# Performance work log

Hardware: AMD Instinct MI355X
Metric: run time of the kernel (lower is better)

Reference implementation:

```python
import jax, jax.numpy as jnp
import numpy as np

G, N = 1024, 40            # graphs, nodes per graph (complete graphs)
SLOPE = 0.1                # leaky relu negative slope
SMAT_IDX = jnp.array([0, 1, 2, 3, 1, 4, 5, 6, 2, 5, 7, 8, 3, 6, 8, 9])


def setup_inputs() -> dict:
    key = jax.random.key(0)
    ks = jax.random.split(key, 24)

    # --- graph structure: G identical complete graphs of N nodes ---
    ii, jj = np.meshgrid(np.arange(N), np.arange(N), indexing="ij")
    mask = ii != jj
    src_l, dst_l = ii[mask], jj[mask]              # directed edges per graph
    offs = (np.arange(G) * N)[:, None]
    edge_index = np.stack([(src_l[None] + offs).ravel(),
                           (dst_l[None] + offs).ravel()]).astype(np.int64)
    iu, ju = np.triu_indices(N, 1)
    M = iu.shape[0]                                 # 780 undirected edges
    ud_edges = np.stack([iu, ju], 1).astype(np.int64)
    edge_map = np.zeros((N, N), np.int64)
    edge_map[iu, ju] = np.arange(M)
    edge_map[ju, iu] = np.arange(M)

    def w(k, shape, fan_in):
        return jax.random.normal(k, shape, jnp.float32) / np.sqrt(fan_in)

    inp = {
        "x": jax.random.normal(ks[0], (G * N, 16), jnp.float32),
        "edge_index": jnp.asarray(edge_index),
        "ud_edges": jnp.asarray(ud_edges),
        "edge_map": jnp.asarray(edge_map),
        # GCN stack 6->32->32->64
        "Wg0": w(ks[1], (6, 32), 6),   "bg0": jnp.zeros((32,), jnp.float32),
        "Wg1": w(ks[2], (32, 32), 32), "bg1": jnp.zeros((32,), jnp.float32),
        "Wg2": w(ks[3], (32, 64), 32), "bg2": jnp.zeros((64,), jnp.float32),
        # node MLP 64->64->64->10
        "Wn0": w(ks[4], (64, 64), 64), "bn0": jnp.zeros((64,), jnp.float32),
        "Wn1": w(ks[5], (64, 64), 64), "bn1": jnp.zeros((64,), jnp.float32),
        "Wn2": w(ks[6], (64, 10), 64), "bn2": jnp.zeros((10,), jnp.float32),
        # edge MLP 64->64->64->10
        "We0": w(ks[7], (64, 64), 64), "be0": jnp.zeros((64,), jnp.float32),
        "We1": w(ks[8], (64, 64), 64), "be1": jnp.zeros((64,), jnp.float32),
        "We2": w(ks[9], (64, 10), 64), "be2": jnp.zeros((10,), jnp.float32),
    }
    return inp


def _forward(x, edge_index, ud_edges, edge_map,
             Wg0, bg0, Wg1, bg1, Wg2, bg2,
             Wn0, bn0, Wn1, bn1, Wn2, bn2,
             We0, be0, We1, be1, We2, be2):
    num_nodes = x.shape[0]
    h = x[:, :6]                                   # node_feature_mode == 1
    src, dst = edge_index[0], edge_index[1]

    # GCN normalization (add_self_loops=False, edge_weight=1)
    deg = jax.ops.segment_sum(jnp.ones(src.shape[0], x.dtype), dst,
                              num_segments=num_nodes)
    dis = jnp.where(deg > 0, jax.lax.rsqrt(jnp.maximum(deg, 1e-12)), 0.0)
    norm = dis[src] * dis[dst]                     # [E]

    def gcn(h, W, b):
        m = (h @ W)[src] * norm[:, None]
        return jax.ops.segment_sum(m, dst, num_segments=num_nodes) + b

    # eval mode: dropout is identity
    h = jax.nn.leaky_relu(gcn(h, Wg0, bg0), SLOPE)
    h = jax.nn.leaky_relu(gcn(h, Wg1, bg1), SLOPE)
    h = gcn(h, Wg2, bg2)                           # [G*N, 64]

    hg = h.reshape(G, N, -1)                       # [G, N, 64]

    def mlp(z, Ws, bs):
        for W, b in zip(Ws[:-1], bs[:-1]):
            z = jax.nn.leaky_relu(z @ W + b, SLOPE)
        return z @ Ws[-1] + bs[-1]

    vp = mlp(hg, [Wn0, Wn1, Wn2], [bn0, bn1, bn2])            # [G, N, 10]
    e = hg[:, ud_edges[:, 0], :] + hg[:, ud_edges[:, 1], :]   # [G, M, 64]
    ep = mlp(e, [We0, We1, We2], [be0, be1, be2])             # [G, M, 10]

    # recover_X: diag blocks smat(vp[i]), off-diag smat(ep[edge_map[i,j]])
    epm = ep[:, edge_map, :]                                  # [G, N, N, 10]
    eye = jnp.eye(N, dtype=bool)[None, :, :, None]
    vecs = jnp.where(eye, vp[:, :, None, :], epm)             # [G, N, N, 10]
    blocks = vecs[..., SMAT_IDX].reshape(G, N, N, 4, 4)
    X = blocks.transpose(0, 1, 3, 2, 4).reshape(G, 4 * N, 4 * N)
    return h, X


def reference(x, edge_index, ud_edges, edge_map,
              Wg0, bg0, Wg1, bg1, Wg2, bg2,
              Wn0, bn0, Wn1, bn1, Wn2, bn2,
              We0, be0, We1, be1, We2, be2):
    return _forward(x, edge_index, ud_edges, edge_map,
                    Wg0, bg0, Wg1, bg1, Wg2, bg2,
                    Wn0, bn0, Wn1, bn1, Wn2, bn2,
                    We0, be0, We1, be1, We2, be2)
```

## Files before the change

### kernel.cpp

```cpp
#include <hip/hip_runtime.h>

#define G_GRAPHS 1024
#define N_NODES  40
#define M_EDGES  780
#define NUM_NODES (G_GRAPHS * N_NODES)
#define H_ELEMS  (NUM_NODES * 64)
#define X_STRIDE 160
#define X_PER_G  25600
#define SLOPE 0.1f

#define PACK_PER_MLP 9216

typedef __bf16 bf16x8 __attribute__((ext_vector_type(8)));
typedef unsigned short us8 __attribute__((ext_vector_type(8)));
typedef float f32x4 __attribute__((ext_vector_type(4)));

__device__ __forceinline__ float lrelu(float v) { return fmaxf(v, SLOPE * v); }
__device__ __forceinline__ unsigned short f2bf(float x) {
    __bf16 b = (__bf16)x;
    return __builtin_bit_cast(unsigned short, b);
}
__device__ __forceinline__ unsigned int pk2bf(float a, float b) {
    return (unsigned int)f2bf(a) | ((unsigned int)f2bf(b) << 16);
}

__global__ __launch_bounds__(256) void k_prep(const float* __restrict__ We0,
                                              const float* __restrict__ We1,
                                              const float* __restrict__ We2,
                                              const float* __restrict__ Wn0,
                                              const float* __restrict__ Wn1,
                                              const float* __restrict__ Wn2,
                                              unsigned short* __restrict__ wp) {
    int t = blockIdx.x * 256 + threadIdx.x;
    int mlp = t / PACK_PER_MLP;
    int o = t - mlp * PACK_PER_MLP;
    const float* W0 = mlp ? Wn0 : We0;
    const float* W1 = mlp ? Wn1 : We1;
    const float* W2 = mlp ? Wn2 : We2;
    float val;
    if (o < 8192) {
        const float* W = (o < 4096) ? W0 : W1;
        int idx = o & 4095;
        int j = idx & 7, l = (idx >> 3) & 63, tt = idx >> 9;
        int kt = tt & 1, mt = tt >> 1;
        int k = kt * 32 + ((l >> 4) & 3) * 8 + j;
        int m = mt * 16 + (l & 15);
        val = W[k * 64 + m];
    } else {
        int idx = o - 8192;
        int j = idx & 7, l = (idx >> 3) & 63, kt = idx >> 9;
        int k = kt * 32 + ((l >> 4) & 3) * 8 + j;
        int m = l & 15;
        val = (m < 10) ? W2[k * 10 + m] : 0.f;
    }
    wp[mlp * PACK_PER_MLP + o] = f2bf(val);
}

struct ChunkRegs {
    bf16x8 A1[4][2];
    bf16x8 A2[4][2];
    bf16x8 A3[2];
    float4 bv0[4];
    float4 bv1[4];
    float  bz[4];
};

__device__ __forceinline__ void run_pair(int R0A, int R0B, int w, int l,
                                         const float4* sh4,
                                         unsigned short* sBA,
                                         unsigned short* sBB,
                                         float* sEP,
                                         const unsigned short* sIJ,
                                         const ChunkRegs& cr) {
    const int nl = l & 15;
    const int rq = (l >> 4) & 3;
    const int rl = l >> 1;
    const int hf2 = l & 1;

    auto decode = [&](int row, int& ii, int& jj, bool& is_e, bool& is_n) {
        is_e = (row < 780);
        is_n = (row >= 800 && row < 840);
        ii = 0; jj = 0;
        if (is_e) {
            unsigned short e = sIJ[row];
            ii = e >> 8; jj = e & 255;
        } else if (is_n) {
            ii = jj = row - 800;
        }
    };
    int iiA, jjA, iiB, jjB; bool ieA, inA, ieB, inB;
    decode(R0A + rl, iiA, jjA, ieA, inA);
    decode(R0B + rl, iiB, jjB, ieB, inB);

    auto ebuild = [&](unsigned short* sB, int ii, int jj, bool is_e) {
        unsigned short tmp[32];
#pragma unroll
        for (int q = 0; q < 8; q++) {
            int u = hf2 * 8 + q;
            float4 a = sh4[ii * 16 + (u ^ ((ii & 7) << 1))];
            if (is_e) {
                float4 bq = sh4[jj * 16 + (u ^ ((jj & 7) << 1))];
                a.x += bq.x; a.y += bq.y; a.z += bq.z; a.w += bq.w;
            }
            tmp[4 * q + 0] = f2bf(a.x); tmp[4 * q + 1] = f2bf(a.y);
            tmp[4 * q + 2] = f2bf(a.z); tmp[4 * q + 3] = f2bf(a.w);
        }
        int r_sb = 32 * w + rl;
#pragma unroll
        for (int q = 0; q < 4; q++) {
            int cs = (hf2 * 4 + q) ^ (r_sb & 7);
            *(us8*)((char*)sB + r_sb * 128 + cs * 16) = *(const us8*)(tmp + 8 * q);
        }
    };
    ebuild(sBA, iiA, jjA, ieA);
    ebuild(sBB, iiB, jjB, ieB);

    auto ZB = [&](const unsigned short* s, int nt, int kt) -> bf16x8 {
        int node = 32 * w + nt * 16 + nl;
        int cs = (kt * 4 + rq) ^ (node & 7);
        return __builtin_bit_cast(bf16x8,
            *(const us8*)((const char*)s + node * 128 + cs * 16));
    };
    auto zstore = [&](unsigned short* s, int mt, int nt, const f32x4& v) {
        int node = 32 * w + nt * 16 + nl;
        int cs = (mt * 2 + (rq >> 1)) ^ (node & 7);
        uint2 u = make_uint2(pk2bf(v[0], v[1]), pk2bf(v[2], v[3]));
        *(uint2*)((char*)s + node * 128 + cs * 16 + (rq & 1) * 8) = u;
    };

    auto gemm_layer = [&](unsigned short* s, const bf16x8 A[4][2],
                          const float4* bv) {
        bf16x8 B[2][2];
#pragma unroll
        for (int nt = 0; nt < 2; nt++)
#pragma unroll
            for (int kt = 0; kt < 2; kt++) B[nt][kt] = ZB(s, nt, kt);
#pragma unroll
        for (int mt = 0; mt < 4; mt++) {
            float4 b = bv[mt];
#pragma unroll
            for (int nt = 0; nt < 2; nt++) {
                f32x4 acc = (f32x4){b.x, b.y, b.z, b.w};
                acc = __builtin_amdgcn_mfma_f32_16x16x32_bf16(A[mt][0], B[nt][0], acc, 0, 0, 0);
                acc = __builtin_amdgcn_mfma_f32_16x16x32_bf16(A[mt][1], B[nt][1], acc, 0, 0, 0);
                f32x4 z;
                z[0] = lrelu(acc[0]); z[1] = lrelu(acc[1]);
                z[2] = lrelu(acc[2]); z[3] = lrelu(acc[3]);
                zstore(s, mt, nt, z);
            }
        }
    };

    gemm_layer(sBA, cr.A1, cr.bv0);
    gemm_layer(sBB, cr.A1, cr.bv0);
    gemm_layer(sBA, cr.A2, cr.bv1);
    gemm_layer(sBB, cr.A2, cr.bv1);

    auto gemm3 = [&](unsigned short* s, int R0) {
        bf16x8 B[2][2];
#pragma unroll
        for (int nt = 0; nt < 2; nt++)
#pragma unroll
            for (int kt = 0; kt < 2; kt++) B[nt][kt] = ZB(s, nt, kt);
#pragma unroll
        for (int nt = 0; nt < 2; nt++) {
            f32x4 acc = (f32x4){cr.bz[0], cr.bz[1], cr.bz[2], cr.bz[3]};
            acc = __builtin_amdgcn_mfma_f32_16x16x32_bf16(cr.A3[0], B[nt][0], acc, 0, 0, 0);
            acc = __builtin_amdgcn_mfma_f32_16x16x32_bf16(cr.A3[1], B[nt][1], acc, 0, 0, 0);
            int rowe = R0 + nt * 16 + nl;
            bool valid = (rowe < 780) || (rowe >= 800 && rowe < 840);
            if (valid && rq < 3) {
                int epr = (rowe < 780) ? rowe : rowe - 20;
                float* p = sEP + epr * 10 + rq * 4;
                *(float2*)p = make_float2(acc[0], acc[1]);
                if (rq < 2)
                    *(float2*)(p + 2) = make_float2(acc[2], acc[3]);
            }
        }
    };
    gemm3(sBA, R0A);
    gemm3(sBB, R0B);
}

__device__ __forceinline__ void run_single(int R0, int w, int l,
                                           const float4* sh4,
                                           unsigned short* sBA,
                                           float* sEP,
                                           const unsigned short* sIJ,
                                           const ChunkRegs& cr) {
    const int nl = l & 15;
    const int rq = (l >> 4) & 3;
    const int rl = l >> 1;
    const int hf2 = l & 1;
    const int row = R0 + rl;

    const bool is_e = (row < 780);
    const bool is_n = (row >= 800 && row < 840);
    int ii = 0, jj = 0;
    if (is_e) {
        unsigned short e = sIJ[row];
        ii = e >> 8; jj = e & 255;
    } else if (is_n) {
        ii = jj = row - 800;
    }

    {
        unsigned short tmp[32];
#pragma unroll
        for (int q = 0; q < 8; q++) {
            int u = hf2 * 8 + q;
            float4 a = sh4[ii * 16 + (u ^ ((ii & 7) << 1))];
            if (is_e) {
                float4 bq = sh4[jj * 16 + (u ^ ((jj & 7) << 1))];
                a.x += bq.x; a.y += bq.y; a.z += bq.z; a.w += bq.w;
            }
            tmp[4 * q + 0] = f2bf(a.x); tmp[4 * q + 1] = f2bf(a.y);
            tmp[4 * q + 2] = f2bf(a.z); tmp[4 * q + 3] = f2bf(a.w);
        }
        int r_sb = 32 * w + rl;
#pragma unroll
        for (int q = 0; q < 4; q++) {
            int cs = (hf2 * 4 + q) ^ (r_sb & 7);
            *(us8*)((char*)sBA + r_sb * 128 + cs * 16) = *(const us8*)(tmp + 8 * q);
        }
    }

    auto ZB = [&](int nt, int kt) -> bf16x8 {
        int node = 32 * w + nt * 16 + nl;
        int cs = (kt * 4 + rq) ^ (node & 7);
        return __builtin_bit_cast(bf16x8,
            *(const us8*)((const char*)sBA + node * 128 + cs * 16));
    };
    auto zstore = [&](int mt, int nt, const f32x4& v) {
        int node = 32 * w + nt * 16 + nl;
        int cs = (mt * 2 + (rq >> 1)) ^ (node & 7);
        uint2 u = make_uint2(pk2bf(v[0], v[1]), pk2bf(v[2], v[3]));
        *(uint2*)((char*)sBA + node * 128 + cs * 16 + (rq & 1) * 8) = u;
    };
    auto gemm_layer = [&](const bf16x8 A[4][2], const float4* bv) {
        bf16x8 B[2][2];
#pragma unroll
        for (int nt = 0; nt < 2; nt++)
#pragma unroll
            for (int kt = 0; kt < 2; kt++) B[nt][kt] = ZB(nt, kt);
#pragma unroll
        for (int mt = 0; mt < 4; mt++) {
            float4 b = bv[mt];
#pragma unroll
            for (int nt = 0; nt < 2; nt++) {
                f32x4 acc = (f32x4){b.x, b.y, b.z, b.w};
                acc = __builtin_amdgcn_mfma_f32_16x16x32_bf16(A[mt][0], B[nt][0], acc, 0, 0, 0);
                acc = __builtin_amdgcn_mfma_f32_16x16x32_bf16(A[mt][1], B[nt][1], acc, 0, 0, 0);
                f32x4 z;
                z[0] = lrelu(acc[0]); z[1] = lrelu(acc[1]);
                z[2] = lrelu(acc[2]); z[3] = lrelu(acc[3]);
                zstore(mt, nt, z);
            }
        }
    };
    gemm_layer(cr.A1, cr.bv0);
    gemm_layer(cr.A2, cr.bv1);
    {
        bf16x8 B[2][2];
#pragma unroll
        for (int nt = 0; nt < 2; nt++)
#pragma unroll
            for (int kt = 0; kt < 2; kt++) B[nt][kt] = ZB(nt, kt);
#pragma unroll
        for (int nt = 0; nt < 2; nt++) {
            f32x4 acc = (f32x4){cr.bz[0], cr.bz[1], cr.bz[2], cr.bz[3]};
            acc = __builtin_amdgcn_mfma_f32_16x16x32_bf16(cr.A3[0], B[nt][0], acc, 0, 0, 0);
            acc = __builtin_amdgcn_mfma_f32_16x16x32_bf16(cr.A3[1], B[nt][1], acc, 0, 0, 0);
            int rowe = R0 + nt * 16 + nl;
            bool valid = (rowe < 780) || (rowe >= 800 && rowe < 840);
            if (valid && rq < 3) {
                int epr = (rowe < 780) ? rowe : rowe - 20;
                float* p = sEP + epr * 10 + rq * 4;
                *(float2*)p = make_float2(acc[0], acc[1]);
                if (rq < 2)
                    *(float2*)(p + 2) = make_float2(acc[2], acc[3]);
            }
        }
    }
}

__global__ __launch_bounds__(256, 2) void k_fused(const float* __restrict__ x,
                                                  const float* __restrict__ Wg0,
                                                  const float* __restrict__ bg0,
                                                  const float* __restrict__ Wg1,
                                                  const float* __restrict__ bg1,
                                                  const float* __restrict__ Wg2,
                                                  const float* __restrict__ bg2,
                                                  const unsigned short* __restrict__ wp,
                                                  const float* __restrict__ be0,
                                                  const float* __restrict__ be1,
                                                  const float* __restrict__ be2,
                                                  const float* __restrict__ bn0,
                                                  const float* __restrict__ bn1,
                                                  const float* __restrict__ bn2,
                                                  float* __restrict__ hout,
                                                  float* __restrict__ X) {
    __shared__ __align__(16) char smem[77368];
    float* sh           = (float*)smem;
    unsigned short* sBA = (unsigned short*)(smem + 10240);
    unsigned short* sBB = (unsigned short*)(smem + 26624);
    float* sEP          = (float*)(smem + 43008);
    unsigned short* sIJ = (unsigned short*)(smem + 75808);
    float* h0  = (float*)smem;
    float* h1  = (float*)(smem + 20480);
    float* h2  = (float*)(smem + 26624);
    float* P   = (float*)(smem + 43008);

    const int g = blockIdx.x;
    const int tid = threadIdx.x;
    const int l = tid & 63;
    const int w = tid >> 6;
    const float inv39 = 1.0f / 39.0f;
    const int c32 = tid & 31;
    const int c64 = tid & 63;
    const int rq = (l >> 4) & 3;

    for (int m = tid; m < 780; m += 256) {
        float tq = 6241.0f - 8.0f * (float)m;
        int i0 = (int)(0.5f * (79.0f - sqrtf(tq)));
        i0 = min(38, max(0, i0));
        int cum = 39 * i0 - ((i0 * (i0 - 1)) >> 1);
        if (cum > m) { --i0; cum = 39 * i0 - ((i0 * (i0 - 1)) >> 1); }
        else if (m - cum >= 39 - i0) { cum += 39 - i0; ++i0; }
        int jj = i0 + 1 + (m - cum);
        sIJ[m] = (unsigned short)((i0 << 8) | jj);
    }

    {
        float w0c[6], w1c[32], w2c[32];
#pragma unroll
        for (int f = 0; f < 6; f++)  w0c[f] = Wg0[f * 32 + c32];
#pragma unroll
        for (int m = 0; m < 32; m++) w1c[m] = Wg1[m * 32 + c32];
#pragma unroll
        for (int m = 0; m < 32; m++) w2c[m] = Wg2[m * 64 + c64];
        const float b0c = bg0[c32];
        const float b1c = bg1[c32];
        const float b2c = bg2[c64];

        if (tid < 240) {
            int n = tid / 6, f = tid - n * 6;
            h0[tid] = x[(g * N_NODES + n) * 16 + f];
        }
        __syncthreads();

        float breg[10];
        const int n0 = tid >> 5;

        {
            float psum = 0.f;
#pragma unroll
            for (int t = 0; t < 5; t++) {
                int n = n0 + 8 * t;
                float s = 0.f;
#pragma unroll
                for (int f = 0; f < 6; f++) s += h0[n * 6 + f] * w0c[f];
                breg[t] = s; psum += s;
            }
            P[n0 * 32 + c32] = psum;
        }
        __syncthreads();
        {
            float s0 = 0.f;
#pragma unroll
            for (int grp = 0; grp < 8; grp++) s0 += P[grp * 32 + c32];
#pragma unroll
            for (int t = 0; t < 5; t++)
                h1[(n0 + 8 * t) * 32 + c32] = lrelu((s0 - breg[t]) * inv39 + b0c);
        }
        __syncthreads();

        {
            float psum = 0.f;
#pragma unroll
            for (int t = 0; t < 5; t++) {
                int n = n0 + 8 * t;
                const float4* hp = (const float4*)(h1 + n * 32);
                float s = 0.f;
#pragma unroll
                for (int q = 0; q < 8; q++) {
                    float4 hv = hp[q];
                    s += hv.x * w1c[4 * q + 0] + hv.y * w1c[4 * q + 1]
                       + hv.z * w1c[4 * q + 2] + hv.w * w1c[4 * q + 3];
                }
                breg[t] = s; psum += s;
            }
            P[n0 * 32 + c32] = psum;
        }
        __syncthreads();
        {
            float s0 = 0.f;
#pragma unroll
            for (int grp = 0; grp < 8; grp++) s0 += P[grp * 32 + c32];
#pragma unroll
            for (int t = 0; t < 5; t++)
                h2[(n0 + 8 * t) * 32 + c32] = lrelu((s0 - breg[t]) * inv39 + b1c);
        }
        __syncthreads();

        const int n02 = tid >> 6;
        {
            float psum = 0.f;
#pragma unroll
            for (int t = 0; t < 10; t++) {
                int n = n02 + 4 * t;
                const float4* hp = (const float4*)(h2 + n * 32);
                float s = 0.f;
#pragma unroll
                for (int q = 0; q < 8; q++) {
                    float4 hv = hp[q];
                    s += hv.x * w2c[4 * q + 0] + hv.y * w2c[4 * q + 1]
                       + hv.z * w2c[4 * q + 2] + hv.w * w2c[4 * q + 3];
                }
                breg[t] = s; psum += s;
            }
            P[n02 * 64 + c64] = psum;
        }
        __syncthreads();
        {
            float s0 = 0.f;
#pragma unroll
            for (int grp = 0; grp < 4; grp++) s0 += P[grp * 64 + c64];
#pragma unroll
            for (int t = 0; t < 10; t++) {
                int n = n02 + 4 * t;
                float v = (s0 - breg[t]) * inv39 + b2c;
                hout[g * N_NODES * 64 + n * 64 + c64] = v;
                int u = c64 >> 2;
                int us = u ^ ((n & 7) << 1);
                sh[n * 64 + us * 4 + (c64 & 3)] = v;
            }
        }
    }
    __syncthreads();

    const float4* sh4 = (const float4*)sh;

    auto WA = [&](const unsigned short* base, int mt, int kt) -> bf16x8 {
        return __builtin_bit_cast(bf16x8,
            *(const us8*)(base + ((mt * 2 + kt) * 64 + l) * 8));
    };
    auto loadW = [&](ChunkRegs& cr, const unsigned short* wb,
                     const float* B0, const float* B1, const float* B2) {
#pragma unroll
        for (int mt = 0; mt < 4; mt++) {
#pragma unroll
            for (int kt = 0; kt < 2; kt++) {
                cr.A1[mt][kt] = WA(wb, mt, kt);
                cr.A2[mt][kt] = WA(wb + 4096, mt, kt);
            }
            cr.bv0[mt] = *(const float4*)(B0 + mt * 16 + rq * 4);
            cr.bv1[mt] = *(const float4*)(B1 + mt * 16 + rq * 4);
        }
        cr.A3[0] = WA(wb + 8192, 0, 0);
        cr.A3[1] = WA(wb + 8192, 0, 1);
#pragma unroll
        for (int k = 0; k < 4; k++) {
            int f = rq * 4 + k;
            cr.bz[k] = (f < 10) ? B2[f] : 0.f;
        }
    };

    ChunkRegs ce;
    loadW(ce, wp, be0, be1, be2);

#pragma unroll
    for (int t = 0; t < 3; t++) {
        int c1 = 2 * w + 8 * t;
        run_pair(32 * c1, 32 * (c1 + 1), w, l, sh4, sBA, sBB, sEP, sIJ, ce);
    }
    if (w == 0) {
        run_single(32 * 24, w, l, sh4, sBA, sEP, sIJ, ce);
    } else if (w == 1) {
        loadW(ce, wp + PACK_PER_MLP, bn0, bn1, bn2);
        run_single(32 * 25, w, l, sh4, sBA, sEP, sIJ, ce);
    } else if (w == 2) {
        loadW(ce, wp + PACK_PER_MLP, bn0, bn1, bn2);
        run_single(32 * 26, w, l, sh4, sBA, sEP, sIJ, ce);
    }

    __syncthreads();

    float* Xg = X + g * X_PER_G;
#pragma unroll
    for (int k = 0; k < 7; k++) {
        int b = k * 256 + tid;
        if (b < 1600) {
            int bi = b / 40;
            int bj = b - bi * 40;
            int ridx;
            if (bi == bj) {
                ridx = 780 + bi;
            } else {
                int mn = min(bi, bj), mx = max(bi, bj);
                ridx = 39 * mn - ((mn * (mn - 1)) >> 1) + (mx - mn - 1);
            }
            const float* ep = sEP + ridx * 10;
            float2 e0 = *(const float2*)(ep + 0);
            float2 e1 = *(const float2*)(ep + 2);
            float2 e2 = *(const float2*)(ep + 4);
            float2 e3 = *(const float2*)(ep + 6);
            float2 e4 = *(const float2*)(ep + 8);
            float f0 = e0.x, f1 = e0.y, f2 = e1.x, f3 = e1.y;
            float f4 = e2.x, f5 = e2.y, f6 = e3.x, f7 = e3.y;
            float f8 = e4.x, f9 = e4.y;
            float4 r0 = make_float4(f0, f1, f2, f3);
            float4 r1 = make_float4(f1, f4, f5, f6);
            float4 r2 = make_float4(f2, f5, f7, f8);
            float4 r3 = make_float4(f3, f6, f8, f9);
            float* p = Xg + (4 * bi) * X_STRIDE + 4 * bj;
            *(float4*)(p + 0 * X_STRIDE) = r0;
            *(float4*)(p + 1 * X_STRIDE) = r1;
            *(float4*)(p + 2 * X_STRIDE) = r2;
            *(float4*)(p + 3 * X_STRIDE) = r3;
        }
    }
}

extern "C" void kernel_launch(void* const* d_in, const int* in_sizes, int n_in,
                              void* d_out, int out_size, void* d_ws, size_t ws_size,
                              hipStream_t stream) {
    const float* x   = (const float*)d_in[0];
    const float* Wg0 = (const float*)d_in[4];
    const float* bg0 = (const float*)d_in[5];
    const float* Wg1 = (const float*)d_in[6];
    const float* bg1 = (const float*)d_in[7];
    const float* Wg2 = (const float*)d_in[8];
    const float* bg2 = (const float*)d_in[9];
    const float* Wn0 = (const float*)d_in[10];
    const float* bn0 = (const float*)d_in[11];
    const float* Wn1 = (const float*)d_in[12];
    const float* bn1 = (const float*)d_in[13];
    const float* Wn2 = (const float*)d_in[14];
    const float* bn2 = (const float*)d_in[15];
    const float* We0 = (const float*)d_in[16];
    const float* be0 = (const float*)d_in[17];
    const float* We1 = (const float*)d_in[18];
    const float* be1 = (const float*)d_in[19];
    const float* We2 = (const float*)d_in[20];
    const float* be2 = (const float*)d_in[21];

    float* hout = (float*)d_out;
    float* X    = hout + H_ELEMS;
    unsigned short* wp = (unsigned short*)d_ws;

    k_prep<<<72, 256, 0, stream>>>(We0, We1, We2, Wn0, Wn1, Wn2, wp);
    k_fused<<<G_GRAPHS, 256, 0, stream>>>(x, Wg0, bg0, Wg1, bg1, Wg2, bg2,
                                          wp, be0, be1, be2, bn0, bn1, bn2,
                                          hout, X);
}
```

Before: 204.3 us.

## Build edge features via one-hot MFMA gather instead of scalar LDS adds

Edge and node inputs to the MLPs were built by reading two rows of h from shared memory, adding them in fp32 and converting to bf16. The new path stores h once as a bf16 MFMA A-operand held in registers. Each row of the B tile becomes a one-hot or two-hot selector vector, and an extra MFMA layer does the gather and add. This replaces many LDS reads and conversions with a few selector writes plus 16 extra MFMAs per chunk, and also shrinks shared memory. The cost is more registers for the hAf fragments and a changed rounding order, since h is rounded to bf16 before the add rather than after.

```diff
diff --git a/kernel.cpp b/kernel.cpp
--- a/kernel.cpp
+++ b/kernel.cpp
@@ -66,7 +66,7 @@
 };
 
 __device__ __forceinline__ void run_pair(int R0A, int R0B, int w, int l,
-                                         const float4* sh4,
+                                         const bf16x8 (&hAf)[4][2],
                                          unsigned short* sBA,
                                          unsigned short* sBB,
                                          float* sEP,
@@ -76,6 +76,7 @@
     const int rq = (l >> 4) & 3;
     const int rl = l >> 1;
     const int hf2 = l & 1;
+    const int r_sb = 32 * w + rl;
 
     auto decode = [&](int row, int& ii, int& jj, bool& is_e, bool& is_n) {
         is_e = (row < 780);
@@ -92,28 +93,27 @@
     decode(R0A + rl, iiA, jjA, ieA, inA);
     decode(R0B + rl, iiB, jjB, ieB, inB);
 
-    auto ebuild = [&](unsigned short* sB, int ii, int jj, bool is_e) {
-        unsigned short tmp[32];
-#pragma unroll
-        for (int q = 0; q < 8; q++) {
-            int u = hf2 * 8 + q;
-            float4 a = sh4[ii * 16 + (u ^ ((ii & 7) << 1))];
-            if (is_e) {
-                float4 bq = sh4[jj * 16 + (u ^ ((jj & 7) << 1))];
-                a.x += bq.x; a.y += bq.y; a.z += bq.z; a.w += bq.w;
-            }
-            tmp[4 * q + 0] = f2bf(a.x); tmp[4 * q + 1] = f2bf(a.y);
-            tmp[4 * q + 2] = f2bf(a.z); tmp[4 * q + 3] = f2bf(a.w);
-        }
-        int r_sb = 32 * w + rl;
+    {
+        us8 z = {};
 #pragma unroll
         for (int q = 0; q < 4; q++) {
             int cs = (hf2 * 4 + q) ^ (r_sb & 7);
-            *(us8*)((char*)sB + r_sb * 128 + cs * 16) = *(const us8*)(tmp + 8 * q);
-        }
-    };
-    ebuild(sBA, iiA, jjA, ieA);
-    ebuild(sBB, iiB, jjB, ieB);
+            *(us8*)((char*)sBA + r_sb * 128 + cs * 16) = z;
+            *(us8*)((char*)sBB + r_sb * 128 + cs * 16) = z;
+        }
+        int kA = hf2 ? jjA : iiA;
+        bool wA = hf2 ? ieA : (ieA || inA);
+        if (wA) {
+            int cs = (kA >> 3) ^ (r_sb & 7);
+            *(unsigned short*)((char*)sBA + r_sb * 128 + cs * 16 + (kA & 7) * 2) = 0x3F80;
+        }
+        int kB = hf2 ? jjB : iiB;
+        bool wB = hf2 ? ieB : (ieB || inB);
+        if (wB) {
+            int cs = (kB >> 3) ^ (r_sb & 7);
+            *(unsigned short*)((char*)sBB + r_sb * 128 + cs * 16 + (kB & 7) * 2) = 0x3F80;
+        }
+    }
 
     auto ZB = [&](const unsigned short* s, int nt, int kt) -> bf16x8 {
         int node = 32 * w + nt * 16 + nl;
@@ -121,12 +121,37 @@
         return __builtin_bit_cast(bf16x8,
             *(const us8*)((const char*)s + node * 128 + cs * 16));
     };
-    auto zstore = [&](unsigned short* s, int mt, int nt, const f32x4& v) {
+    auto zstore_raw = [&](unsigned short* s, int mt, int nt, const f32x4& v) {
         int node = 32 * w + nt * 16 + nl;
         int cs = (mt * 2 + (rq >> 1)) ^ (node & 7);
         uint2 u = make_uint2(pk2bf(v[0], v[1]), pk2bf(v[2], v[3]));
         *(uint2*)((char*)s + node * 128 + cs * 16 + (rq & 1) * 8) = u;
     };
+    auto zstore = [&](unsigned short* s, int mt, int nt, const f32x4& v) {
+        f32x4 z;
+        z[0] = lrelu(v[0]); z[1] = lrelu(v[1]);
+        z[2] = lrelu(v[2]); z[3] = lrelu(v[3]);
+        zstore_raw(s, mt, nt, z);
+    };
+
+    auto gemm0 = [&](unsigned short* s) {
+        bf16x8 B[2][2];
+#pragma unroll
+        for (int nt = 0; nt < 2; nt++)
+#pragma unroll
+            for (int kt = 0; kt < 2; kt++) B[nt][kt] = ZB(s, nt, kt);
+#pragma unroll
+        for (int mt = 0; mt < 4; mt++)
+#pragma unroll
+            for (int nt = 0; nt < 2; nt++) {
+                f32x4 acc = (f32x4){0.f, 0.f, 0.f, 0.f};
+                acc = __builtin_amdgcn_mfma_f32_16x16x32_bf16(hAf[mt][0], B[nt][0], acc, 0, 0, 0);
+                acc = __builtin_amdgcn_mfma_f32_16x16x32_bf16(hAf[mt][1], B[nt][1], acc, 0, 0, 0);
+                zstore_raw(s, mt, nt, acc);
+            }
+    };
+    gemm0(sBA);
+    gemm0(sBB);
 
     auto gemm_layer = [&](unsigned short* s, const bf16x8 A[4][2],
                           const float4* bv) {
@@ -143,10 +168,7 @@
                 f32x4 acc = (f32x4){b.x, b.y, b.z, b.w};
                 acc = __builtin_amdgcn_mfma_f32_16x16x32_bf16(A[mt][0], B[nt][0], acc, 0, 0, 0);
                 acc = __builtin_amdgcn_mfma_f32_16x16x32_bf16(A[mt][1], B[nt][1], acc, 0, 0, 0);
-                f32x4 z;
-                z[0] = lrelu(acc[0]); z[1] = lrelu(acc[1]);
-                z[2] = lrelu(acc[2]); z[3] = lrelu(acc[3]);
-                zstore(s, mt, nt, z);
+                zstore(s, mt, nt, acc);
             }
         }
     };
@@ -183,7 +205,7 @@
 }
 
 __device__ __forceinline__ void run_single(int R0, int w, int l,
-                                           const float4* sh4,
+                                           const bf16x8 (&hAf)[4][2],
                                            unsigned short* sBA,
                                            float* sEP,
                                            const unsigned short* sIJ,
@@ -192,6 +214,7 @@
     const int rq = (l >> 4) & 3;
     const int rl = l >> 1;
     const int hf2 = l & 1;
+    const int r_sb = 32 * w + rl;
     const int row = R0 + rl;
 
     const bool is_e = (row < 780);
@@ -205,23 +228,17 @@
     }
 
     {
-        unsigned short tmp[32];
-#pragma unroll
-        for (int q = 0; q < 8; q++) {
-            int u = hf2 * 8 + q;
-            float4 a = sh4[ii * 16 + (u ^ ((ii & 7) << 1))];
-            if (is_e) {
-                float4 bq = sh4[jj * 16 + (u ^ ((jj & 7) << 1))];
-                a.x += bq.x; a.y += bq.y; a.z += bq.z; a.w += bq.w;
-            }
-            tmp[4 * q + 0] = f2bf(a.x); tmp[4 * q + 1] = f2bf(a.y);
-            tmp[4 * q + 2] = f2bf(a.z); tmp[4 * q + 3] = f2bf(a.w);
-        }
-        int r_sb = 32 * w + rl;
+        us8 z = {};
 #pragma unroll
         for (int q = 0; q < 4; q++) {
             int cs = (hf2 * 4 + q) ^ (r_sb & 7);
-            *(us8*)((char*)sBA + r_sb * 128 + cs * 16) = *(const us8*)(tmp + 8 * q);
+            *(us8*)((char*)sBA + r_sb * 128 + cs * 16) = z;
+        }
+        int kk = hf2 ? jj : ii;
+        bool wr = hf2 ? is_e : (is_e || is_n);
+        if (wr) {
+            int cs = (kk >> 3) ^ (r_sb & 7);
+            *(unsigned short*)((char*)sBA + r_sb * 128 + cs * 16 + (kk & 7) * 2) = 0x3F80;
         }
     }
 
@@ -231,12 +248,30 @@
         return __builtin_bit_cast(bf16x8,
             *(const us8*)((const char*)sBA + node * 128 + cs * 16));
     };
-    auto zstore = [&](int mt, int nt, const f32x4& v) {
+    auto zstore_raw = [&](int mt, int nt, const f32x4& v) {
         int node = 32 * w + nt * 16 + nl;
         int cs = (mt * 2 + (rq >> 1)) ^ (node & 7);
         uint2 u = make_uint2(pk2bf(v[0], v[1]), pk2bf(v[2], v[3]));
         *(uint2*)((char*)sBA + node * 128 + cs * 16 + (rq & 1) * 8) = u;
     };
+
+    {
+        bf16x8 B[2][2];
+#pragma unroll
+        for (int nt = 0; nt < 2; nt++)
+#pragma unroll
+            for (int kt = 0; kt < 2; kt++) B[nt][kt] = ZB(nt, kt);
+#pragma unroll
+        for (int mt = 0; mt < 4; mt++)
+#pragma unroll
+            for (int nt = 0; nt < 2; nt++) {
+                f32x4 acc = (f32x4){0.f, 0.f, 0.f, 0.f};
+                acc = __builtin_amdgcn_mfma_f32_16x16x32_bf16(hAf[mt][0], B[nt][0], acc, 0, 0, 0);
+                acc = __builtin_amdgcn_mfma_f32_16x16x32_bf16(hAf[mt][1], B[nt][1], acc, 0, 0, 0);
+                zstore_raw(mt, nt, acc);
+            }
+    }
+
     auto gemm_layer = [&](const bf16x8 A[4][2], const float4* bv) {
         bf16x8 B[2][2];
 #pragma unroll
@@ -254,7 +289,7 @@
                 f32x4 z;
                 z[0] = lrelu(acc[0]); z[1] = lrelu(acc[1]);
                 z[2] = lrelu(acc[2]); z[3] = lrelu(acc[3]);
-                zstore(mt, nt, z);
+                zstore_raw(mt, nt, z);
             }
         }
     };
@@ -300,16 +335,16 @@
                                                   const float* __restrict__ bn2,
                                                   float* __restrict__ hout,
                                                   float* __restrict__ X) {
-    __shared__ __align__(16) char smem[77368];
-    float* sh           = (float*)smem;
-    unsigned short* sBA = (unsigned short*)(smem + 10240);
-    unsigned short* sBB = (unsigned short*)(smem + 26624);
-    float* sEP          = (float*)(smem + 43008);
-    unsigned short* sIJ = (unsigned short*)(smem + 75808);
+    __shared__ __align__(16) char smem[75320];
+    unsigned short* hAu = (unsigned short*)smem;
+    unsigned short* sBA = (unsigned short*)(smem + 8192);
+    unsigned short* sBB = (unsigned short*)(smem + 24576);
+    float* sEP          = (float*)(smem + 40960);
+    unsigned short* sIJ = (unsigned short*)(smem + 73760);
     float* h0  = (float*)smem;
-    float* h1  = (float*)(smem + 20480);
-    float* h2  = (float*)(smem + 26624);
-    float* P   = (float*)(smem + 43008);
+    float* h1  = (float*)(smem + 8192);
+    float* h2  = (float*)(smem + 13312);
+    float* P   = (float*)(smem + 40960);
 
     const int g = blockIdx.x;
     const int tid = threadIdx.x;
@@ -330,6 +365,12 @@
         int jj = i0 + 1 + (m - cum);
         sIJ[m] = (unsigned short)((i0 << 8) | jj);
     }
+    if (tid < 192) {
+        int mt = tid / 48;
+        int lz = 16 + (tid % 48);
+        us8 z = {};
+        *(us8*)((char*)smem + ((mt * 2 + 1) * 64 + lz) * 16) = z;
+    }
 
     {
         float w0c[6], w1c[32], w2c[32];
@@ -426,20 +467,27 @@
             float s0 = 0.f;
 #pragma unroll
             for (int grp = 0; grp < 4; grp++) s0 += P[grp * 64 + c64];
+            const int mt = c64 >> 4, nln = c64 & 15;
 #pragma unroll
             for (int t = 0; t < 10; t++) {
                 int n = n02 + 4 * t;
                 float v = (s0 - breg[t]) * inv39 + b2c;
                 hout[g * N_NODES * 64 + n * 64 + c64] = v;
-                int u = c64 >> 2;
-                int us = u ^ ((n & 7) << 1);
-                sh[n * 64 + us * 4 + (c64 & 3)] = v;
+                int kt = n >> 5, rqn = (n >> 3) & 3, jn = n & 7;
+                int ln = rqn * 16 + nln;
+                hAu[((mt * 2 + kt) * 64 + ln) * 8 + jn] = f2bf(v);
             }
         }
     }
     __syncthreads();
 
-    const float4* sh4 = (const float4*)sh;
+    bf16x8 hAf[4][2];
+#pragma unroll
+    for (int mt = 0; mt < 4; mt++)
+#pragma unroll
+        for (int kt = 0; kt < 2; kt++)
+            hAf[mt][kt] = __builtin_bit_cast(bf16x8,
+                *(const us8*)(hAu + ((mt * 2 + kt) * 64 + l) * 8));
 
     auto WA = [&](const unsigned short* base, int mt, int kt) -> bf16x8 {
         return __builtin_bit_cast(bf16x8,
@@ -472,16 +520,16 @@
 #pragma unroll
     for (int t = 0; t < 3; t++) {
         int c1 = 2 * w + 8 * t;
-        run_pair(32 * c1, 32 * (c1 + 1), w, l, sh4, sBA, sBB, sEP, sIJ, ce);
+        run_pair(32 * c1, 32 * (c1 + 1), w, l, hAf, sBA, sBB, sEP, sIJ, ce);
     }
     if (w == 0) {
-        run_single(32 * 24, w, l, sh4, sBA, sEP, sIJ, ce);
+        run_single(32 * 24, w, l, hAf, sBA, sEP, sIJ, ce);
     } else if (w == 1) {
         loadW(ce, wp + PACK_PER_MLP, bn0, bn1, bn2);
-        run_single(32 * 25, w, l, sh4, sBA, sEP, sIJ, ce);
+        run_single(32 * 25, w, l, hAf, sBA, sEP, sIJ, ce);
     } else if (w == 2) {
         loadW(ce, wp + PACK_PER_MLP, bn0, bn1, bn2);
-        run_single(32 * 26, w, l, sh4, sBA, sEP, sIJ, ce);
+        run_single(32 * 26, w, l, hAf, sBA, sEP, sIJ, ce);
     }
 
     __syncthreads();
```

After: 202.4 us. No clear change (-0.9%).

## Fold edge sum into first MLP layer via linearity and store h as bf16

Applied to the files above, without the earlier changes.

The explicit edge-feature build (h[i]+h[j] converted to bf16 and staged in LDS) is removed. The first edge-MLP layer now reads h[i] and h[j] bf16 fragments straight from a swizzled bf16 copy of h and sums W*h_i + W*h_j by chaining two extra MFMAs into the accumulator. A zero row at index 40 handles node and padding rows, and LeakyReLU moves into the store. This cuts LDS traffic and conversion work at the cost of twice the MFMAs in layer 1 and rounding h before the sum, and the shared-memory layout shrinks.

```diff
diff --git a/kernel.cpp b/kernel.cpp
--- a/kernel.cpp
+++ b/kernel.cpp
@@ -65,8 +65,15 @@
     float  bz[4];
 };
 
+__device__ __forceinline__ void dec2(const unsigned short* sIJ, int row,
+                                     int& i, int& j) {
+    if (row < 780) { int e = sIJ[row]; i = e >> 8; j = e & 255; }
+    else if (row >= 800 && row < 840) { i = row - 800; j = 40; }
+    else { i = 40; j = 40; }
+}
+
 __device__ __forceinline__ void run_pair(int R0A, int R0B, int w, int l,
-                                         const float4* sh4,
+                                         const unsigned short* hBu,
                                          unsigned short* sBA,
                                          unsigned short* sBB,
                                          float* sEP,
@@ -74,47 +81,17 @@
                                          const ChunkRegs& cr) {
     const int nl = l & 15;
     const int rq = (l >> 4) & 3;
-    const int rl = l >> 1;
-    const int hf2 = l & 1;
-
-    auto decode = [&](int row, int& ii, int& jj, bool& is_e, bool& is_n) {
-        is_e = (row < 780);
-        is_n = (row >= 800 && row < 840);
-        ii = 0; jj = 0;
-        if (is_e) {
-            unsigned short e = sIJ[row];
-            ii = e >> 8; jj = e & 255;
-        } else if (is_n) {
-            ii = jj = row - 800;
-        }
-    };
-    int iiA, jjA, iiB, jjB; bool ieA, inA, ieB, inB;
-    decode(R0A + rl, iiA, jjA, ieA, inA);
-    decode(R0B + rl, iiB, jjB, ieB, inB);
-
-    auto ebuild = [&](unsigned short* sB, int ii, int jj, bool is_e) {
-        unsigned short tmp[32];
-#pragma unroll
-        for (int q = 0; q < 8; q++) {
-            int u = hf2 * 8 + q;
-            float4 a = sh4[ii * 16 + (u ^ ((ii & 7) << 1))];
-            if (is_e) {
-                float4 bq = sh4[jj * 16 + (u ^ ((jj & 7) << 1))];
-                a.x += bq.x; a.y += bq.y; a.z += bq.z; a.w += bq.w;
-            }
-            tmp[4 * q + 0] = f2bf(a.x); tmp[4 * q + 1] = f2bf(a.y);
-            tmp[4 * q + 2] = f2bf(a.z); tmp[4 * q + 3] = f2bf(a.w);
-        }
-        int r_sb = 32 * w + rl;
-#pragma unroll
-        for (int q = 0; q < 4; q++) {
-            int cs = (hf2 * 4 + q) ^ (r_sb & 7);
-            *(us8*)((char*)sB + r_sb * 128 + cs * 16) = *(const us8*)(tmp + 8 * q);
-        }
-    };
-    ebuild(sBA, iiA, jjA, ieA);
-    ebuild(sBB, iiB, jjB, ieB);
-
+
+    int iA[2], jA[2], iB[2], jB[2];
+    dec2(sIJ, R0A + nl, iA[0], jA[0]);
+    dec2(sIJ, R0A + 16 + nl, iA[1], jA[1]);
+    dec2(sIJ, R0B + nl, iB[0], jB[0]);
+    dec2(sIJ, R0B + 16 + nl, iB[1], jB[1]);
+
+    auto BH = [&](int i, int kt) -> bf16x8 {
+        int u = (kt * 4 + rq) ^ (i & 7);
+        return __builtin_bit_cast(bf16x8, *(const us8*)(hBu + i * 64 + u * 8));
+    };
     auto ZB = [&](const unsigned short* s, int nt, int kt) -> bf16x8 {
         int node = 32 * w + nt * 16 + nl;
         int cs = (kt * 4 + rq) ^ (node & 7);
@@ -124,37 +101,57 @@
     auto zstore = [&](unsigned short* s, int mt, int nt, const f32x4& v) {
         int node = 32 * w + nt * 16 + nl;
         int cs = (mt * 2 + (rq >> 1)) ^ (node & 7);
-        uint2 u = make_uint2(pk2bf(v[0], v[1]), pk2bf(v[2], v[3]));
+        uint2 u = make_uint2(pk2bf(lrelu(v[0]), lrelu(v[1])),
+                             pk2bf(lrelu(v[2]), lrelu(v[3])));
         *(uint2*)((char*)s + node * 128 + cs * 16 + (rq & 1) * 8) = u;
     };
 
-    auto gemm_layer = [&](unsigned short* s, const bf16x8 A[4][2],
-                          const float4* bv) {
-        bf16x8 B[2][2];
+    auto gemm1 = [&](unsigned short* s, const int (&iN)[2], const int (&jN)[2]) {
+        bf16x8 Bi[2][2], Bj[2][2];
 #pragma unroll
         for (int nt = 0; nt < 2; nt++)
 #pragma unroll
-            for (int kt = 0; kt < 2; kt++) B[nt][kt] = ZB(s, nt, kt);
+            for (int kt = 0; kt < 2; kt++) {
+                Bi[nt][kt] = BH(iN[nt], kt);
+                Bj[nt][kt] = BH(jN[nt], kt);
+            }
 #pragma unroll
         for (int mt = 0; mt < 4; mt++) {
-            float4 b = bv[mt];
+            float4 b = cr.bv0[mt];
 #pragma unroll
             for (int nt = 0; nt < 2; nt++) {
                 f32x4 acc = (f32x4){b.x, b.y, b.z, b.w};
-                acc = __builtin_amdgcn_mfma_f32_16x16x32_bf16(A[mt][0], B[nt][0], acc, 0, 0, 0);
-                acc = __builtin_amdgcn_mfma_f32_16x16x32_bf16(A[mt][1], B[nt][1], acc, 0, 0, 0);
-                f32x4 z;
-                z[0] = lrelu(acc[0]); z[1] = lrelu(acc[1]);
-                z[2] = lrelu(acc[2]); z[3] = lrelu(acc[3]);
-                zstore(s, mt, nt, z);
-            }
-        }
-    };
-
-    gemm_layer(sBA, cr.A1, cr.bv0);
-    gemm_layer(sBB, cr.A1, cr.bv0);
-    gemm_layer(sBA, cr.A2, cr.bv1);
-    gemm_layer(sBB, cr.A2, cr.bv1);
+                acc = __builtin_amdgcn_mfma_f32_16x16x32_bf16(cr.A1[mt][0], Bi[nt][0], acc, 0, 0, 0);
+                acc = __builtin_amdgcn_mfma_f32_16x16x32_bf16(cr.A1[mt][1], Bi[nt][1], acc, 0, 0, 0);
+                acc = __builtin_amdgcn_mfma_f32_16x16x32_bf16(cr.A1[mt][0], Bj[nt][0], acc, 0, 0, 0);
+                acc = __builtin_amdgcn_mfma_f32_16x16x32_bf16(cr.A1[mt][1], Bj[nt][1], acc, 0, 0, 0);
+                zstore(s, mt, nt, acc);
+            }
+        }
+    };
+    gemm1(sBA, iA, jA);
+    gemm1(sBB, iB, jB);
+
+    auto gemm2 = [&](unsigned short* s) {
+        bf16x8 B[2][2];
+#pragma unroll
+        for (int nt = 0; nt < 2; nt++)
+#pragma unroll
+            for (int kt = 0; kt < 2; kt++) B[nt][kt] = ZB(s, nt, kt);
+#pragma unroll
+        for (int mt = 0; mt < 4; mt++) {
+            float4 b = cr.bv1[mt];
+#pragma unroll
+            for (int nt = 0; nt < 2; nt++) {
+                f32x4 acc = (f32x4){b.x, b.y, b.z, b.w};
+                acc = __builtin_amdgcn_mfma_f32_16x16x32_bf16(cr.A2[mt][0], B[nt][0], acc, 0, 0, 0);
+                acc = __builtin_amdgcn_mfma_f32_16x16x32_bf16(cr.A2[mt][1], B[nt][1], acc, 0, 0, 0);
+                zstore(s, mt, nt, acc);
+            }
+        }
+    };
+    gemm2(sBA);
+    gemm2(sBB);
 
     auto gemm3 = [&](unsigned short* s, int R0) {
         bf16x8 B[2][2];
@@ -183,48 +180,22 @@
 }
 
 __device__ __forceinline__ void run_single(int R0, int w, int l,
-                                           const float4* sh4,
+                                           const unsigned short* hBu,
                                            unsigned short* sBA,
                                            float* sEP,
                                            const unsigned short* sIJ,
                                            const ChunkRegs& cr) {
     const int nl = l & 15;
     const int rq = (l >> 4) & 3;
-    const int rl = l >> 1;
-    const int hf2 = l & 1;
-    const int row = R0 + rl;
-
-    const bool is_e = (row < 780);
-    const bool is_n = (row >= 800 && row < 840);
-    int ii = 0, jj = 0;
-    if (is_e) {
-        unsigned short e = sIJ[row];
-        ii = e >> 8; jj = e & 255;
-    } else if (is_n) {
-        ii = jj = row - 800;
-    }
-
-    {
-        unsigned short tmp[32];
-#pragma unroll
-        for (int q = 0; q < 8; q++) {
-            int u = hf2 * 8 + q;
-            float4 a = sh4[ii * 16 + (u ^ ((ii & 7) << 1))];
-            if (is_e) {
-                float4 bq = sh4[jj * 16 + (u ^ ((jj & 7) << 1))];
-                a.x += bq.x; a.y += bq.y; a.z += bq.z; a.w += bq.w;
-            }
-            tmp[4 * q + 0] = f2bf(a.x); tmp[4 * q + 1] = f2bf(a.y);
-            tmp[4 * q + 2] = f2bf(a.z); tmp[4 * q + 3] = f2bf(a.w);
-        }
-        int r_sb = 32 * w + rl;
-#pragma unroll
-        for (int q = 0; q < 4; q++) {
-            int cs = (hf2 * 4 + q) ^ (r_sb & 7);
-            *(us8*)((char*)sBA + r_sb * 128 + cs * 16) = *(const us8*)(tmp + 8 * q);
-        }
-    }
-
+
+    int iN[2], jN[2];
+    dec2(sIJ, R0 + nl, iN[0], jN[0]);
+    dec2(sIJ, R0 + 16 + nl, iN[1], jN[1]);
+
+    auto BH = [&](int i, int kt) -> bf16x8 {
+        int u = (kt * 4 + rq) ^ (i & 7);
+        return __builtin_bit_cast(bf16x8, *(const us8*)(hBu + i * 64 + u * 8));
+    };
     auto ZB = [&](int nt, int kt) -> bf16x8 {
         int node = 32 * w + nt * 16 + nl;
         int cs = (kt * 4 + rq) ^ (node & 7);
@@ -234,32 +205,52 @@
     auto zstore = [&](int mt, int nt, const f32x4& v) {
         int node = 32 * w + nt * 16 + nl;
         int cs = (mt * 2 + (rq >> 1)) ^ (node & 7);
-        uint2 u = make_uint2(pk2bf(v[0], v[1]), pk2bf(v[2], v[3]));
+        uint2 u = make_uint2(pk2bf(lrelu(v[0]), lrelu(v[1])),
+                             pk2bf(lrelu(v[2]), lrelu(v[3])));
         *(uint2*)((char*)sBA + node * 128 + cs * 16 + (rq & 1) * 8) = u;
     };
-    auto gemm_layer = [&](const bf16x8 A[4][2], const float4* bv) {
-        bf16x8 B[2][2];
+
+    {
+        bf16x8 Bi[2][2], Bj[2][2];
 #pragma unroll
         for (int nt = 0; nt < 2; nt++)
 #pragma unroll
-            for (int kt = 0; kt < 2; kt++) B[nt][kt] = ZB(nt, kt);
+            for (int kt = 0; kt < 2; kt++) {
+                Bi[nt][kt] = BH(iN[nt], kt);
+                Bj[nt][kt] = BH(jN[nt], kt);
+            }
 #pragma unroll
         for (int mt = 0; mt < 4; mt++) {
-            float4 b = bv[mt];
+            float4 b = cr.bv0[mt];
 #pragma unroll
             for (int nt = 0; nt < 2; nt++) {
                 f32x4 acc = (f32x4){b.x, b.y, b.z, b.w};
-                acc = __builtin_amdgcn_mfma_f32_16x16x32_bf16(A[mt][0], B[nt][0], acc, 0, 0, 0);
-                acc = __builtin_amdgcn_mfma_f32_16x16x32_bf16(A[mt][1], B[nt][1], acc, 0, 0, 0);
-                f32x4 z;
-                z[0] = lrelu(acc[0]); z[1] = lrelu(acc[1]);
-                z[2] = lrelu(acc[2]); z[3] = lrelu(acc[3]);
-                zstore(mt, nt, z);
-            }
-        }
-    };
-    gemm_layer(cr.A1, cr.bv0);
-    gemm_layer(cr.A2, cr.bv1);
+                acc = __builtin_amdgcn_mfma_f32_16x16x32_bf16(cr.A1[mt][0], Bi[nt][0], acc, 0, 0, 0);
+                acc = __builtin_amdgcn_mfma_f32_16x16x32_bf16(cr.A1[mt][1], Bi[nt][1], acc, 0, 0, 0);
+                acc = __builtin_amdgcn_mfma_f32_16x16x32_bf16(cr.A1[mt][0], Bj[nt][0], acc, 0, 0, 0);
+                acc = __builtin_amdgcn_mfma_f32_16x16x32_bf16(cr.A1[mt][1], Bj[nt][1], acc, 0, 0, 0);
+                zstore(mt, nt, acc);
+            }
+        }
+    }
+    {
+        bf16x8 B[2][2];
+#pragma unroll
+        for (int nt = 0; nt < 2; nt++)
+#pragma unroll
+            for (int kt = 0; kt < 2; kt++) B[nt][kt] = ZB(nt, kt);
+#pragma unroll
+        for (int mt = 0; mt < 4; mt++) {
+            float4 b = cr.bv1[mt];
+#pragma unroll
+            for (int nt = 0; nt < 2; nt++) {
+                f32x4 acc = (f32x4){b.x, b.y, b.z, b.w};
+                acc = __builtin_amdgcn_mfma_f32_16x16x32_bf16(cr.A2[mt][0], B[nt][0], acc, 0, 0, 0);
+                acc = __builtin_amdgcn_mfma_f32_16x16x32_bf16(cr.A2[mt][1], B[nt][1], acc, 0, 0, 0);
+                zstore(mt, nt, acc);
+            }
+        }
+    }
     {
         bf16x8 B[2][2];
 #pragma unroll
@@ -300,16 +291,16 @@
                                                   const float* __restrict__ bn2,
                                                   float* __restrict__ hout,
                                                   float* __restrict__ X) {
-    __shared__ __align__(16) char smem[77368];
-    float* sh           = (float*)smem;
-    unsigned short* sBA = (unsigned short*)(smem + 10240);
-    unsigned short* sBB = (unsigned short*)(smem + 26624);
-    float* sEP          = (float*)(smem + 43008);
-    unsigned short* sIJ = (unsigned short*)(smem + 75808);
+    __shared__ __align__(16) char smem[73376];
+    unsigned short* hBu = (unsigned short*)smem;
+    unsigned short* sIJ = (unsigned short*)(smem + 6144);
+    unsigned short* sBA = (unsigned short*)(smem + 7808);
+    unsigned short* sBB = (unsigned short*)(smem + 24192);
+    float* sEP          = (float*)(smem + 40576);
     float* h0  = (float*)smem;
-    float* h1  = (float*)(smem + 20480);
-    float* h2  = (float*)(smem + 26624);
-    float* P   = (float*)(smem + 43008);
+    float* h1  = (float*)(smem + 7808);
+    float* h2  = (float*)(smem + 12928);
+    float* P   = (float*)(smem + 40576);
 
     const int g = blockIdx.x;
     const int tid = threadIdx.x;
@@ -330,6 +321,10 @@
         int jj = i0 + 1 + (m - cum);
         sIJ[m] = (unsigned short)((i0 << 8) | jj);
     }
+    if (tid < 64) {
+        us8 z = {};
+        *(us8*)(hBu + (40 + (tid >> 3)) * 64 + (tid & 7) * 8) = z;
+    }
 
     {
         float w0c[6], w1c[32], w2c[32];
@@ -431,15 +426,12 @@
                 int n = n02 + 4 * t;
                 float v = (s0 - breg[t]) * inv39 + b2c;
                 hout[g * N_NODES * 64 + n * 64 + c64] = v;
-                int u = c64 >> 2;
-                int us = u ^ ((n & 7) << 1);
-                sh[n * 64 + us * 4 + (c64 & 3)] = v;
+                int u = (c64 >> 3) ^ (n & 7);
+                hBu[n * 64 + u * 8 + (c64 & 7)] = f2bf(v);
             }
         }
     }
     __syncthreads();
-
-    const float4* sh4 = (const float4*)sh;
 
     auto WA = [&](const unsigned short* base, int mt, int kt) -> bf16x8 {
         return __builtin_bit_cast(bf16x8,
@@ -472,16 +464,16 @@
 #pragma unroll
     for (int t = 0; t < 3; t++) {
         int c1 = 2 * w + 8 * t;
-        run_pair(32 * c1, 32 * (c1 + 1), w, l, sh4, sBA, sBB, sEP, sIJ, ce);
+        run_pair(32 * c1, 32 * (c1 + 1), w, l, hBu, sBA, sBB, sEP, sIJ, ce);
     }
     if (w == 0) {
-        run_single(32 * 24, w, l, sh4, sBA, sEP, sIJ, ce);
+        run_single(32 * 24, w, l, hBu, sBA, sEP, sIJ, ce);
     } else if (w == 1) {
         loadW(ce, wp + PACK_PER_MLP, bn0, bn1, bn2);
-        run_single(32 * 25, w, l, sh4, sBA, sEP, sIJ, ce);
+        run_single(32 * 25, w, l, hBu, sBA, sEP, sIJ, ce);
     } else if (w == 2) {
         loadW(ce, wp + PACK_PER_MLP, bn0, bn1, bn2);
-        run_single(32 * 26, w, l, sh4, sBA, sEP, sIJ, ce);
+        run_single(32 * 26, w, l, hBu, sBA, sEP, sIJ, ce);
     }
 
     __syncthreads();
```

New measurement: 194.9 us. 1.05x faster.
